# Kernel optimization log

Measured on AMD Instinct MI355X. Metric: run time of the kernel, lower is better.

## Reference

```python
import jax, jax.numpy as jnp
import numpy as np

EXP = 1.4  # cp/cv exponent in the pressure diagnostic

# 2-point stencil primitives (equivalent to the tiny conv3d calls in the torch code)
def bar_x(X):      return 0.5 * (X[:, :, 1:] + X[:, :, :-1])
def dlt_x(X, dx):  return (X[:, :, 1:] - X[:, :, :-1]) / dx
def bar_y(X):      return 0.5 * (X[:, 1:, :] + X[:, :-1, :])
def dlt_y(X, dy):  return (X[:, 1:, :] - X[:, :-1, :]) / dy
def bar_z(X):      return 0.5 * (X[1:] + X[:-1])
def dlt_z(X, dz):  return (X[1:] - X[:-1]) / dz
def pad_x(X):      return jnp.pad(X, ((0, 0), (0, 0), (1, 1)), mode='wrap')      # periodic
def pad_y(X):      return jnp.pad(X, ((0, 0), (1, 1), (0, 0)), mode='wrap')      # periodic
def pad_z(X):      return jnp.pad(X, ((1, 1), (0, 0), (0, 0)))                   # Dirichlet 0 (torch code zeroes top/surface args)


def rhs(U, V, W, Theta, Mu, Phi, dx, dy, dz, PREF, Rd, g):
    u = U / bar_x(pad_x(Mu))                       # (Nz,Ny,Nx+1)
    v = V / bar_y(pad_y(Mu))                       # (Nz,Ny+1,Nx)
    w = W / bar_z(Mu)                              # (Nz-1,Ny,Nx)
    alpha = -dlt_z(pad_z(Phi), dz) / Mu            # (Nz,Ny,Nx)
    theta = Theta / Mu
    p = PREF * (Rd * theta / PREF / alpha) ** EXP
    omega = -w * g / bar_z(alpha) / bar_z(Mu)
    Omega = omega * bar_z(Mu)                      # (Nz-1,Ny,Nx)

    R_U = (-dlt_x(bar_x(pad_x(U)) * bar_x(pad_x(u)), dx)
           - dlt_y(bar_x(pad_x(V)) * bar_y(pad_y(u)), dy)
           - dlt_z(bar_x(pad_x(pad_z(Omega))) * bar_z(pad_z(u)), dz))
    R_V = (-dlt_x(bar_y(pad_y(U)) * bar_x(pad_x(v)), dx)
           - dlt_y(bar_y(pad_y(V)) * bar_y(pad_y(v)), dy)
           - dlt_z(bar_y(pad_y(pad_z(Omega))) * bar_z(pad_z(v)), dz))
    R_W = (-dlt_x(bar_z(U) * bar_x(pad_x(w)), dx)
           - dlt_y(bar_z(V) * bar_y(pad_y(w)), dy)
           - dlt_z(bar_z(pad_z(Omega)) * bar_z(pad_z(w)), dz))
    R_Theta = (-dlt_x(U * bar_x(pad_x(theta)), dx)
               - dlt_y(V * bar_y(pad_y(theta)), dy)
               - dlt_z(pad_z(Omega) * bar_z(pad_z(theta)), dz))
    R_Phi = (-bar_z(bar_x(u)) * dlt_x(bar_x(pad_x(Phi)), dx)
             - bar_z(bar_y(v)) * dlt_y(bar_y(pad_y(Phi)), dy)
             - Omega * dlt_z(bar_z(pad_z(Phi)), dz))
    R_Mu = -dlt_x(U, dx) - dlt_y(V, dy) - dlt_z(pad_z(Omega), dz)

    R_U = R_U + (-bar_x(pad_x(Mu)) * bar_x(pad_x(alpha)) * dlt_x(pad_x(p), dx)
                 - dlt_z(bar_x(bar_z(pad_x(pad_z(p)))), dz) * dlt_x(pad_x(bar_z(pad_z(Phi))), dx))
    R_V = R_V + (-bar_y(pad_y(Mu)) * bar_y(pad_y(alpha)) * dlt_y(pad_y(p), dy)
                 - dlt_z(bar_y(bar_z(pad_y(pad_z(p)))), dz) * dlt_y(pad_y(bar_z(pad_z(Phi))), dy))
    R_W = R_W + g * (dlt_z(p, dz) - bar_z(Mu))
    R_Phi = R_Phi + g * w
    return R_U, R_V, R_W, R_Theta, R_Mu, R_Phi


def rk3_step(U, V, W, Theta, Mu, Phi, dt, dx, dy, dz, PREF, Rd, g):
    rU, rV, rW, rT, rM, rP = rhs(U, V, W, Theta, Mu, Phi, dx, dy, dz, PREF, Rd, g)
    U1, V1, W1 = U + dt * rU / 3, V + dt * rV / 3, W + dt * rW / 3
    T1, M1, P1 = Theta + dt * rT / 3, Mu + dt * rM / 3, Phi + dt * rP / 3
    rU, rV, rW, rT, rM, rP = rhs(U1, V1, W1, T1, M1, P1, dx, dy, dz, PREF, Rd, g)
    U2, V2, W2 = U + dt * rU / 2, V + dt * rV / 2, W + dt * rW / 2
    T2, M2, P2 = Theta + dt * rT / 2, Mu + dt * rM / 2, Phi + dt * rP / 2
    rU, rV, rW, rT, rM, rP = rhs(U2, V2, W2, T2, M2, P2, dx, dy, dz, PREF, Rd, g)
    return (U + dt * rU, V + dt * rV, W + dt * rW,
            Theta + dt * rT, Mu + dt * rM, Phi + dt * rP)


def setup_inputs() -> dict:
    Nz, Ny, Nx = 40, 256, 256
    key = jax.random.key(0)
    k1, k2, k3, k4, k5, k6, k7 = jax.random.split(key, 7)
    dx = dy = dz = 1.0
    dt, PREF, Rd, g = 1e-3, 1.0, 1.0, 0.1

    # Column-mass: positive, O(1)
    Mu = (1.0 + 0.1 * jax.random.uniform(k1, (Nz, Ny, Nx))).astype(jnp.float32)
    # Block-signed vertical diff profile: magnitudes bounded away from 0,
    # distinct block magnitudes so bar_z(alpha) never vanishes at the sign flip.
    base = jnp.where(jnp.arange(Nz) < 30, 1.0, -3.0)[:, None, None]
    d = (base * (1.0 + 0.1 * jax.random.uniform(k2, (Nz, Ny, Nx)))).astype(jnp.float32)
    Phi = jnp.cumsum(d, axis=0)[: Nz - 1]          # (Nz-1,Ny,Nx)
    # alpha exactly as the model will compute it
    alpha = -dlt_z(pad_z(Phi), dz) / Mu            # (Nz,Ny,Nx), sign-definite per block
    s = 1.0 + 0.2 * jax.random.uniform(k3, (Nz, Ny, Nx))
    Theta = ((PREF / Rd) * Mu * alpha * s).astype(jnp.float32)  # theta/alpha = s > 0 -> p well-defined

    U = (0.01 * jax.random.normal(k4, (Nz, Ny, Nx + 1))).astype(jnp.float32)
    V = (0.01 * jax.random.normal(k5, (Nz, Ny + 1, Nx))).astype(jnp.float32)
    W = (0.01 * jax.random.normal(k6, (Nz - 1, Ny, Nx))).astype(jnp.float32)

    bnd = jax.random.uniform(k7, (6, 1, Ny, Nx), dtype=jnp.float32)
    return {"U": U, "V": V, "W": W, "Theta": Theta, "Mu": Mu, "Phi": Phi,
            "Phi_t": bnd[0], "Phi_s": bnd[1], "theta_t": bnd[2], "theta_s": bnd[3],
            "P_t": bnd[4], "P_s": bnd[5],
            "dx": dx, "dy": dy, "dz": dz, "dt": dt, "PREF": PREF, "Rd": Rd, "g": g}


def reference(U, V, W, Theta, Mu, Phi, Phi_t, Phi_s, theta_t, theta_s, P_t, P_s,
              dx, dy, dz, dt, PREF, Rd, g):
    # Phi_t/Phi_s/theta_t/theta_s/P_t/P_s are ignored: the torch pad_z always
    # overwrites top/surface with zeros (faithful to the original code).
    return rk3_step(U, V, W, Theta, Mu, Phi, dt, dx, dy, dz, PREF, Rd, g)
```

## Files before the change

### kernel.cpp

```cpp
#include <hip/hip_runtime.h>
#include <math.h>

#define NZ 40
#define NY 256
#define NX 256
#define NUX 257
#define NYX (NY*NX)
#define KU (NY*NUX)
#define KV ((NY+1)*NX)
#define NUT (NZ*KU)
#define NVT (NZ*KV)
#define NCT (NZ*NYX)
#define NWT ((NZ-1)*NYX)
#define NBLK (NUX*NZ)
#define NHALF (NUT+NVT+NWT+3*NCT+NWT)

typedef _Float16 h16;

__device__ __forceinline__ int ICc(int k,int j,int i){ return (k*NY+j)*NX+i; }
__device__ __forceinline__ int IU (int k,int j,int i){ return (k*NY+j)*NUX+i; }
__device__ __forceinline__ int IV (int k,int j,int i){ return (k*(NY+1)+j)*NX+i; }

__device__ __forceinline__ float fdiv(float a, float b){
  return a * __builtin_amdgcn_rcpf(b);
}
__device__ __forceinline__ float ldh(const h16* __restrict__ a, int idx){
  return (float)a[idx];
}

__global__ __launch_bounds__(256) void diag_all(
    const float* __restrict__ Us, const float* __restrict__ Vs, const float* __restrict__ Ws,
    const float* __restrict__ Ts, const float* __restrict__ Ms, const float* __restrict__ Ps,
    h16* __restrict__ ud, h16* __restrict__ vd, h16* __restrict__ wd,
    h16* __restrict__ thd, h16* __restrict__ ald, h16* __restrict__ pd,
    h16* __restrict__ Omd,
    const float* __restrict__ dzp, const float* __restrict__ PREFp,
    const float* __restrict__ Rdp, const float* __restrict__ gp)
{
  const int i = threadIdx.x;
  const int j = blockIdx.x;
  const int k = blockIdx.y;
  const float rdz = 1.f/(*dzp);
  const float PREF = *PREFp, Rd = *Rdp, g = *gp;
  const float invP = 1.f/PREF;

  const int jj  = j & 255;
  const int jm1 = (j+255) & 255;

  {
    float mjm = Ms[(k*NY+jm1)*NX+i];
    float mjj = Ms[(k*NY+jj )*NX+i];
    const int o = IV(k,j,i);
    vd[o] = (h16)fdiv(Vs[o], 0.5f*(mjm+mjj));
  }

  if (j < NY) {
    const int b = (k*NY+j)*NX;
    float mi  = Ms[b+i];
    float mim = Ms[b+((i+255)&255)];
    ud[IU(k,j,i)] = (h16)fdiv(Us[IU(k,j,i)], 0.5f*(mim+mi));
    if (i == 255) {
      ud[IU(k,j,256)] = (h16)fdiv(Us[IU(k,j,256)], 0.5f*(Ms[b+255]+Ms[b+0]));
    }

    const int c = b + i;
    float mu   = mi;
    float phim = (k>0)    ? Ps[c-NYX] : 0.f;
    float phik = (k<NZ-1) ? Ps[c]     : 0.f;
    float al   = -((phik-phim)*rdz)*__builtin_amdgcn_rcpf(mu);
    float th   = fdiv(Ts[c], mu);
    float x    = Rd*th*invP*__builtin_amdgcn_rcpf(al);
    pd[c]  = (h16)(PREF*__builtin_amdgcn_exp2f(1.4f*__builtin_amdgcn_logf(x)));
    ald[c] = (h16)al;
    thd[c] = (h16)th;
    if (k < NZ-1) {
      float mup  = Ms[c+NYX];
      float phip = (k+1<NZ-1) ? Ps[c+NYX] : 0.f;
      float alp  = -((phip-phik)*rdz)*__builtin_amdgcn_rcpf(mup);
      float muz  = 0.5f*(mu+mup);
      wd[c]  = (h16)fdiv(Ws[c], muz);
      Omd[c] = (h16)(-Ws[c]*g*__builtin_amdgcn_rcpf(muz*(0.5f*(al+alp))));
    }
  }
}

__global__ __launch_bounds__(256,8) void rhs_update(
    const float* __restrict__ Us, const float* __restrict__ Vs,
    const float* __restrict__ Ms, const float* __restrict__ Ps,
    const h16* __restrict__ ud, const h16* __restrict__ vd, const h16* __restrict__ wd,
    const h16* __restrict__ thd, const h16* __restrict__ ald, const h16* __restrict__ pd,
    const h16* __restrict__ Omd,
    const float* __restrict__ Ub, const float* __restrict__ Vb, const float* __restrict__ Wb,
    const float* __restrict__ Tb, const float* __restrict__ Mb, const float* __restrict__ Pb,
    float* __restrict__ Uo, float* __restrict__ Vo, float* __restrict__ Wo,
    float* __restrict__ To, float* __restrict__ Mo, float* __restrict__ Po,
    const float* __restrict__ dxp, const float* __restrict__ dyp, const float* __restrict__ dzp,
    const float* __restrict__ dtp, const float* __restrict__ gp, float cmul)
{
  const int bid = blockIdx.x;
  const int nb  = (bid & 7)*(NBLK/8) + (bid >> 3);
  const int j   = nb / NZ;
  const int k   = nb - NZ*j;
  const int i   = threadIdx.x;

  const float rdx = 1.f/(*dxp), rdy = 1.f/(*dyp), rdz = 1.f/(*dzp);
  const float g = *gp;
  const float c = (*dtp)*cmul;

  const int jj  = j & 255;
  const int jm1 = (j+255) & 255;
  const int jp1c= (j+1) & 255;
  const int im1 = (i+255) & 255;
  const int ip1 = (i+1) & 255;

  auto ru_val = [&](int iu, int iW, int iE)->float {
    const int ii_  = iu & 255;
    const int iim1 = (iu+255) & 255;
    const int bU   = k*KU + j*NUX;

    float ui0 = ldh(ud,bU+iu), uim = ldh(ud,bU+iW), uip = ldh(ud,bU+iE);
    float Uim = Us[bU+iW], Ui0 = Us[bU+iu], Uip = Us[bU+iE];
    float t1 = -(0.25f*(Ui0+Uip)*(ui0+uip) - 0.25f*(Uim+Ui0)*(uim+ui0))*rdx;

    float Vx0 = 0.5f*(Vs[IV(k,j  ,iim1)] + Vs[IV(k,j  ,ii_)]);
    float uy0 = 0.5f*(ldh(ud,IU(k,jm1,iu)) + ui0);
    float Vx1 = 0.5f*(Vs[IV(k,j+1,iim1)] + Vs[IV(k,j+1,ii_)]);
    float uy1 = 0.5f*(ui0 + ldh(ud,IU(k,jp1c,iu)));
    float t2 = -(Vx1*uy1 - Vx0*uy0)*rdy;

    float Omx0 = (k==0)   ? 0.f : 0.5f*(ldh(Omd,ICc(k-1,j,iim1))+ldh(Omd,ICc(k-1,j,ii_)));
    float uz0  = (k==0)   ? 0.5f*ui0 : 0.5f*(ldh(ud,IU(k-1,j,iu))+ui0);
    float Omx1 = (k+1==NZ)? 0.f : 0.5f*(ldh(Omd,ICc(k,j,iim1))+ldh(Omd,ICc(k,j,ii_)));
    float uz1  = (k+1==NZ)? 0.5f*ui0 : 0.5f*(ui0+ldh(ud,IU(k+1,j,iu)));
    float t3 = -(Omx1*uz1 - Omx0*uz0)*rdz;

    float Mux = 0.5f*(Ms[ICc(k,j,iim1)]+Ms[ICc(k,j,ii_)]);
    float alx = 0.5f*(ldh(ald,ICc(k,j,iim1))+ldh(ald,ICc(k,j,ii_)));
    float pt1 = -Mux*alx*(ldh(pd,ICc(k,j,ii_))-ldh(pd,ICc(k,j,iim1)))*rdx;

    auto pzf = [&](int m, int x)->float {
      if (m==0)  return 0.5f*ldh(pd,ICc(0,j,x));
      if (m==NZ) return 0.5f*ldh(pd,ICc(NZ-1,j,x));
      return 0.5f*(ldh(pd,ICc(m-1,j,x))+ldh(pd,ICc(m,j,x)));
    };
    float A = (0.5f*(pzf(k+1,iim1)+pzf(k+1,ii_)) - 0.5f*(pzf(k,iim1)+pzf(k,ii_)))*rdz;
    auto Phzf = [&](int x)->float {
      if (k==0)    return 0.5f*Ps[ICc(0,j,x)];
      if (k==NZ-1) return 0.5f*Ps[ICc(NZ-2,j,x)];
      return 0.5f*(Ps[ICc(k-1,j,x)]+Ps[ICc(k,j,x)]);
    };
    float B = (Phzf(ii_)-Phzf(iim1))*rdx;
    return t1+t2+t3+pt1 + (-A*B);
  };

  if (j < NY) {
    const int iW = i ? (i-1) : 256;
    float rU = ru_val(i, iW, i+1);
    const int o = IU(k,j,i);
    Uo[o] = Ub[o] + c*rU;
    if (i == 255) {
      float rUe = ru_val(256, 255, 0);
      const int oe = IU(k,j,256);
      Uo[oe] = Ub[oe] + c*rUe;
    }
  }

  {
    const int jN = (j==0)   ? 256 : j-1;
    const int jS = (j==256) ? 0   : j+1;
    float vj0 = ldh(vd,IV(k,j,i));
    float vjm = ldh(vd,IV(k,jN,i));
    float vjp = ldh(vd,IV(k,jS,i));
    float Vjm = Vs[IV(k,jN,i)], Vj0 = Vs[IV(k,j,i)], Vjp = Vs[IV(k,jS,i)];
    float t2 = -(0.25f*(Vj0+Vjp)*(vj0+vjp) - 0.25f*(Vjm+Vj0)*(vjm+vj0))*rdy;

    float Uy0 = 0.5f*(Us[IU(k,jm1,i  )] + Us[IU(k,jj,i  )]);
    float vx0 = 0.5f*(ldh(vd,IV(k,j,im1)) + vj0);
    float Uy1 = 0.5f*(Us[IU(k,jm1,i+1)] + Us[IU(k,jj,i+1)]);
    float vx1 = 0.5f*(vj0 + ldh(vd,IV(k,j,ip1)));
    float t1 = -(Uy1*vx1 - Uy0*vx0)*rdx;

    float Omy0 = (k==0)   ? 0.f : 0.5f*(ldh(Omd,ICc(k-1,jm1,i))+ldh(Omd,ICc(k-1,jj,i)));
    float vz0  = (k==0)   ? 0.5f*vj0 : 0.5f*(ldh(vd,IV(k-1,j,i))+vj0);
    float Omy1 = (k+1==NZ)? 0.f : 0.5f*(ldh(Omd,ICc(k,jm1,i))+ldh(Omd,ICc(k,jj,i)));
    float vz1  = (k+1==NZ)? 0.5f*vj0 : 0.5f*(vj0+ldh(vd,IV(k+1,j,i)));
    float t3 = -(Omy1*vz1 - Omy0*vz0)*rdz;

    float Muy = 0.5f*(Ms[ICc(k,jm1,i)]+Ms[ICc(k,jj,i)]);
    float aly = 0.5f*(ldh(ald,ICc(k,jm1,i))+ldh(ald,ICc(k,jj,i)));
    float pt1 = -Muy*aly*(ldh(pd,ICc(k,jj,i))-ldh(pd,ICc(k,jm1,i)))*rdy;

    auto pzfy = [&](int m, int y)->float {
      if (m==0)  return 0.5f*ldh(pd,ICc(0,y,i));
      if (m==NZ) return 0.5f*ldh(pd,ICc(NZ-1,y,i));
      return 0.5f*(ldh(pd,ICc(m-1,y,i))+ldh(pd,ICc(m,y,i)));
    };
    float A = (0.5f*(pzfy(k+1,jm1)+pzfy(k+1,jj)) - 0.5f*(pzfy(k,jm1)+pzfy(k,jj)))*rdz;
    auto Phzfy = [&](int y)->float {
      if (k==0)    return 0.5f*Ps[ICc(0,y,i)];
      if (k==NZ-1) return 0.5f*Ps[ICc(NZ-2,y,i)];
      return 0.5f*(Ps[ICc(k-1,y,i)]+Ps[ICc(k,y,i)]);
    };
    float B = (Phzfy(jj)-Phzfy(jm1))*rdy;
    float pt2 = -A*B;

    const int o = IV(k,j,i);
    Vo[o] = Vb[o] + c*(t1+t2+t3+pt1+pt2);
  }

  if (j < NY) {
    const int cc = ICc(k,j,i);

    float th0 = ldh(thd,cc);
    float thx0 = 0.5f*(ldh(thd,ICc(k,j,im1))+th0);
    float thx1 = 0.5f*(th0+ldh(thd,ICc(k,j,ip1)));
    float s1 = -(Us[IU(k,j,i+1)]*thx1 - Us[IU(k,j,i)]*thx0)*rdx;
    float thy0 = 0.5f*(ldh(thd,ICc(k,jm1,i))+th0);
    float thy1 = 0.5f*(th0+ldh(thd,ICc(k,jp1c,i)));
    float s2 = -(Vs[IV(k,j+1,i)]*thy1 - Vs[IV(k,j,i)]*thy0)*rdy;
    float Om0 = (k==0)    ? 0.f : ldh(Omd,ICc(k-1,j,i));
    float Om1 = (k+1==NZ) ? 0.f : ldh(Omd,cc);
    float thz0 = (k==0)    ? 0.5f*th0 : 0.5f*(ldh(thd,ICc(k-1,j,i))+th0);
    float thz1 = (k+1==NZ) ? 0.5f*th0 : 0.5f*(th0+ldh(thd,ICc(k+1,j,i)));
    float s3 = -(Om1*thz1 - Om0*thz0)*rdz;
    To[cc] = Tb[cc] + c*(s1+s2+s3);

    float rmu = -(Us[IU(k,j,i+1)]-Us[IU(k,j,i)])*rdx
                -(Vs[IV(k,j+1,i)]-Vs[IV(k,j,i)])*rdy
                -(Om1-Om0)*rdz;
    Mo[cc] = Mb[cc] + c*rmu;

    if (k < NZ-1) {
      float w0 = ldh(wd,cc);
      float Uz0 = 0.5f*(Us[IU(k,j,i  )]+Us[IU(k+1,j,i  )]);
      float Uz1 = 0.5f*(Us[IU(k,j,i+1)]+Us[IU(k+1,j,i+1)]);
      float wx0 = 0.5f*(ldh(wd,ICc(k,j,im1))+w0);
      float wx1 = 0.5f*(w0+ldh(wd,ICc(k,j,ip1)));
      float q1 = -(Uz1*wx1 - Uz0*wx0)*rdx;
      float Vz0 = 0.5f*(Vs[IV(k,j  ,i)]+Vs[IV(k+1,j  ,i)]);
      float Vz1 = 0.5f*(Vs[IV(k,j+1,i)]+Vs[IV(k+1,j+1,i)]);
      float wy0 = 0.5f*(ldh(wd,ICc(k,jm1,i))+w0);
      float wy1 = 0.5f*(w0+ldh(wd,ICc(k,jp1c,i)));
      float q2 = -(Vz1*wy1 - Vz0*wy0)*rdy;
      float Omz0 = (k==0)      ? 0.5f*ldh(Omd,ICc(0,j,i))    : 0.5f*(ldh(Omd,ICc(k-1,j,i))+ldh(Omd,cc));
      float wz0  = (k==0)      ? 0.5f*w0 : 0.5f*(ldh(wd,ICc(k-1,j,i))+w0);
      float Omz1 = (k+1==NZ-1) ? 0.5f*ldh(Omd,ICc(NZ-2,j,i)) : 0.5f*(ldh(Omd,cc)+ldh(Omd,ICc(k+1,j,i)));
      float wz1  = (k+1==NZ-1) ? 0.5f*w0 : 0.5f*(w0+ldh(wd,ICc(k+1,j,i)));
      float q3 = -(Omz1*wz1 - Omz0*wz0)*rdz;
      float pw = g*((ldh(pd,ICc(k+1,j,i))-ldh(pd,cc))*rdz - 0.5f*(Ms[cc]+Ms[ICc(k+1,j,i)]));
      Wo[cc] = Wb[cc] + c*(q1+q2+q3+pw);

      float ux0 = 0.5f*(ldh(ud,IU(k  ,j,i))+ldh(ud,IU(k  ,j,i+1)));
      float ux1 = 0.5f*(ldh(ud,IU(k+1,j,i))+ldh(ud,IU(k+1,j,i+1)));
      float uzx = 0.5f*(ux0+ux1);
      float dPhx = 0.5f*(Ps[ICc(k,j,ip1)]-Ps[ICc(k,j,im1)])*rdx;
      float vy0 = 0.5f*(ldh(vd,IV(k  ,j,i))+ldh(vd,IV(k  ,j+1,i)));
      float vy1 = 0.5f*(ldh(vd,IV(k+1,j,i))+ldh(vd,IV(k+1,j+1,i)));
      float vzy = 0.5f*(vy0+vy1);
      float dPhy = 0.5f*(Ps[ICc(k,jp1c,i)]-Ps[ICc(k,jm1,i)])*rdy;
      float Phz0 = (k==0)      ? 0.5f*Ps[ICc(0,j,i)]    : 0.5f*(Ps[ICc(k-1,j,i)]+Ps[cc]);
      float Phz1 = (k+1==NZ-1) ? 0.5f*Ps[ICc(NZ-2,j,i)] : 0.5f*(Ps[cc]+Ps[ICc(k+1,j,i)]);
      float p3 = -ldh(Omd,cc)*(Phz1-Phz0)*rdz;
      Po[cc] = Pb[cc] + c*(-uzx*dPhx - vzy*dPhy + p3 + g*w0);
    }
  }
}

extern "C" void kernel_launch(void* const* d_in, const int* in_sizes, int n_in,
                              void* d_out, int out_size, void* d_ws, size_t ws_size,
                              hipStream_t stream)
{
  const float* U = (const float*)d_in[0];
  const float* V = (const float*)d_in[1];
  const float* W = (const float*)d_in[2];
  const float* T = (const float*)d_in[3];
  const float* M = (const float*)d_in[4];
  const float* P = (const float*)d_in[5];
  const float* dxp  = (const float*)d_in[12];
  const float* dyp  = (const float*)d_in[13];
  const float* dzp  = (const float*)d_in[14];
  const float* dtp  = (const float*)d_in[15];
  const float* PREFp= (const float*)d_in[16];
  const float* Rdp  = (const float*)d_in[17];
  const float* gp   = (const float*)d_in[18];

  h16* hw = (h16*)d_ws;
  h16* ud  = hw;         h16* vd  = ud +NUT;  h16* wd = vd +NVT;
  h16* thd = wd +NWT;    h16* ald = thd+NCT;  h16* pd = ald+NCT;
  h16* Omd = pd +NCT;
  float* S = (float*)(hw + NHALF);
  float* SU=S; float* SV=SU+NUT; float* SW=SV+NVT; float* ST=SW+NWT; float* SM=ST+NCT; float* SP=SM+NCT;

  float* o = (float*)d_out;
  float* OU=o; float* OV=OU+NUT; float* OW=OV+NVT; float* OT=OW+NWT; float* OM=OT+NCT; float* OP=OM+NCT;

  dim3 dblk(256,1,1), dgrd(NUX, NZ, 1);
  dim3 rblk(256,1,1), rgrd(NBLK, 1, 1);

  auto stage = [&](const float* sU,const float* sV,const float* sW,
                   const float* sT,const float* sM,const float* sP,
                   float* oU,float* oV,float* oW,float* oT,float* oM,float* oP,
                   float cmul){
    hipLaunchKernelGGL(diag_all, dgrd, dblk, 0, stream,
                       sU,sV,sW,sT,sM,sP, ud,vd,wd,thd,ald,pd,Omd, dzp,PREFp,Rdp,gp);
    hipLaunchKernelGGL(rhs_update, rgrd, rblk, 0, stream,
                       sU,sV,sM,sP, ud,vd,wd,thd,ald,pd,Omd,
                       U,V,W,T,M,P, oU,oV,oW,oT,oM,oP,
                       dxp,dyp,dzp,dtp,gp, cmul);
  };

  stage(U,V,W,T,M,P,          OU,OV,OW,OT,OM,OP, 1.f/3.f);
  stage(OU,OV,OW,OT,OM,OP,    SU,SV,SW,ST,SM,SP, 0.5f   );
  stage(SU,SV,SW,ST,SM,SP,    OU,OV,OW,OT,OM,OP, 1.f    );
}
```

Baseline: 311.7 us.

## Stage neighbor stencil rows in LDS and lower rhs_update occupancy target

Each block now cooperatively loads every neighbor row it needs (the half-precision u, v, w, theta, p, Omega and alpha fields plus the float Phi and Mu rows) into shared memory once, then computes all stencil terms from LDS. This replaces repeated, partly shifted global loads. The k==0 and k==NZ-1 branches disappear because out-of-range rows are stored as zeros. The launch-bounds minimum-blocks hint also drops from 8 to 6 to relax register pressure. In exchange it adds a block-wide barrier and about 40 staging loads per thread before any compute, which may serialize memory latency that was previously overlapped.

```diff
diff --git a/kernel.cpp b/kernel.cpp
--- a/kernel.cpp
+++ b/kernel.cpp
@@ -84,7 +84,7 @@
   }
 }
 
-__global__ __launch_bounds__(256,8) void rhs_update(
+__global__ __launch_bounds__(256,6) void rhs_update(
     const float* __restrict__ Us, const float* __restrict__ Vs,
     const float* __restrict__ Ms, const float* __restrict__ Ps,
     const h16* __restrict__ ud, const h16* __restrict__ vd, const h16* __restrict__ wd,
@@ -107,49 +107,84 @@
   const float g = *gp;
   const float c = (*dtp)*cmul;
 
-  const int jj  = j & 255;
-  const int jm1 = (j+255) & 255;
-  const int jp1c= (j+1) & 255;
-  const int im1 = (i+255) & 255;
-  const int ip1 = (i+1) & 255;
+  const int jj   = j & 255;
+  const int jm1  = (j+255) & 255;
+  const int jp1m = (j+1) & 255;
+  const int im1  = (i+255) & 255;
+  const int ip1  = (i+1) & 255;
+  const int jN   = (j==0)   ? 256 : j-1;
+  const int jS   = (j==256) ? 0   : j+1;
+
+  __shared__ h16  Lud[5][258];
+  __shared__ h16  Lvd[6][256];
+  __shared__ h16  Lwd[5][256];
+  __shared__ h16  Lth[5][256];
+  __shared__ h16  Lpd[6][256];
+  __shared__ h16  LOm[5][256];
+  __shared__ h16  Lal[2][256];
+  __shared__ float LPs[6][256];
+  __shared__ float LMs[3][256];
+
+#define STC(dst,src,kk,jr,kmax) dst[i] = ((unsigned)(kk)<(unsigned)(kmax)) ? src[((kk)*NY+(jr))*NX+i] : (h16)0.f
+#define STF(dst,src,kk,jr,kmax) dst[i] = ((unsigned)(kk)<(unsigned)(kmax)) ? src[((kk)*NY+(jr))*NX+i] : 0.f
+#define STU(dst,kk,jr) do{ bool v_=((unsigned)(kk)<(unsigned)NZ); \
+    dst[i] = v_ ? ud[((kk)*NY+(jr))*NUX+i] : (h16)0.f; \
+    if (i==0) dst[256] = v_ ? ud[((kk)*NY+(jr))*NUX+256] : (h16)0.f; }while(0)
+#define STV(dst,kk,jr) dst[i] = ((unsigned)(kk)<(unsigned)NZ) ? vd[((kk)*(NY+1)+(jr))*NX+i] : (h16)0.f
+
+  STU(Lud[0],k,  jm1); STU(Lud[1],k,  jj ); STU(Lud[2],k,  jp1m);
+  STU(Lud[3],k-1,jj ); STU(Lud[4],k+1,jj );
+  STV(Lvd[0],k,  jN ); STV(Lvd[1],k,  j  ); STV(Lvd[2],k,  jS );
+  STV(Lvd[3],k-1,j  ); STV(Lvd[4],k+1,j  ); STV(Lvd[5],k+1,jS );
+  STC(Lwd[0],wd,k,  jm1,NZ-1); STC(Lwd[1],wd,k,  jj ,NZ-1); STC(Lwd[2],wd,k,  jp1m,NZ-1);
+  STC(Lwd[3],wd,k-1,jj ,NZ-1); STC(Lwd[4],wd,k+1,jj ,NZ-1);
+  STC(Lth[0],thd,k,  jm1,NZ); STC(Lth[1],thd,k,  jj ,NZ); STC(Lth[2],thd,k,  jp1m,NZ);
+  STC(Lth[3],thd,k-1,jj ,NZ); STC(Lth[4],thd,k+1,jj ,NZ);
+  STC(Lpd[0],pd,k-1,jj ,NZ); STC(Lpd[1],pd,k,  jj ,NZ); STC(Lpd[2],pd,k+1,jj ,NZ);
+  STC(Lpd[3],pd,k-1,jm1,NZ); STC(Lpd[4],pd,k,  jm1,NZ); STC(Lpd[5],pd,k+1,jm1,NZ);
+  STC(LOm[0],Omd,k-1,jj ,NZ-1); STC(LOm[1],Omd,k,  jj ,NZ-1); STC(LOm[2],Omd,k+1,jj ,NZ-1);
+  STC(LOm[3],Omd,k-1,jm1,NZ-1); STC(LOm[4],Omd,k,  jm1,NZ-1);
+  Lal[0][i] = ald[(k*NY+jj )*NX+i];
+  Lal[1][i] = ald[(k*NY+jm1)*NX+i];
+  STF(LPs[0],Ps,k-1,jj ,NZ-1); STF(LPs[1],Ps,k,  jj ,NZ-1); STF(LPs[2],Ps,k+1,jj ,NZ-1);
+  STF(LPs[3],Ps,k,  jm1,NZ-1); STF(LPs[4],Ps,k,  jp1m,NZ-1); STF(LPs[5],Ps,k-1,jm1,NZ-1);
+  STF(LMs[0],Ms,k,  jm1,NZ); STF(LMs[1],Ms,k,  jj ,NZ); STF(LMs[2],Ms,k+1,jj ,NZ);
+
+  __syncthreads();
 
   auto ru_val = [&](int iu, int iW, int iE)->float {
     const int ii_  = iu & 255;
     const int iim1 = (iu+255) & 255;
     const int bU   = k*KU + j*NUX;
 
-    float ui0 = ldh(ud,bU+iu), uim = ldh(ud,bU+iW), uip = ldh(ud,bU+iE);
+    float ui0 = (float)Lud[1][iu], uim = (float)Lud[1][iW], uip = (float)Lud[1][iE];
     float Uim = Us[bU+iW], Ui0 = Us[bU+iu], Uip = Us[bU+iE];
     float t1 = -(0.25f*(Ui0+Uip)*(ui0+uip) - 0.25f*(Uim+Ui0)*(uim+ui0))*rdx;
 
     float Vx0 = 0.5f*(Vs[IV(k,j  ,iim1)] + Vs[IV(k,j  ,ii_)]);
-    float uy0 = 0.5f*(ldh(ud,IU(k,jm1,iu)) + ui0);
+    float uy0 = 0.5f*((float)Lud[0][iu] + ui0);
     float Vx1 = 0.5f*(Vs[IV(k,j+1,iim1)] + Vs[IV(k,j+1,ii_)]);
-    float uy1 = 0.5f*(ui0 + ldh(ud,IU(k,jp1c,iu)));
+    float uy1 = 0.5f*(ui0 + (float)Lud[2][iu]);
     float t2 = -(Vx1*uy1 - Vx0*uy0)*rdy;
 
-    float Omx0 = (k==0)   ? 0.f : 0.5f*(ldh(Omd,ICc(k-1,j,iim1))+ldh(Omd,ICc(k-1,j,ii_)));
-    float uz0  = (k==0)   ? 0.5f*ui0 : 0.5f*(ldh(ud,IU(k-1,j,iu))+ui0);
-    float Omx1 = (k+1==NZ)? 0.f : 0.5f*(ldh(Omd,ICc(k,j,iim1))+ldh(Omd,ICc(k,j,ii_)));
-    float uz1  = (k+1==NZ)? 0.5f*ui0 : 0.5f*(ui0+ldh(ud,IU(k+1,j,iu)));
+    float Omx0 = 0.5f*((float)LOm[0][iim1]+(float)LOm[0][ii_]);
+    float uz0  = 0.5f*((float)Lud[3][iu] + ui0);
+    float Omx1 = 0.5f*((float)LOm[1][iim1]+(float)LOm[1][ii_]);
+    float uz1  = 0.5f*(ui0 + (float)Lud[4][iu]);
     float t3 = -(Omx1*uz1 - Omx0*uz0)*rdz;
 
-    float Mux = 0.5f*(Ms[ICc(k,j,iim1)]+Ms[ICc(k,j,ii_)]);
-    float alx = 0.5f*(ldh(ald,ICc(k,j,iim1))+ldh(ald,ICc(k,j,ii_)));
-    float pt1 = -Mux*alx*(ldh(pd,ICc(k,j,ii_))-ldh(pd,ICc(k,j,iim1)))*rdx;
-
-    auto pzf = [&](int m, int x)->float {
-      if (m==0)  return 0.5f*ldh(pd,ICc(0,j,x));
-      if (m==NZ) return 0.5f*ldh(pd,ICc(NZ-1,j,x));
-      return 0.5f*(ldh(pd,ICc(m-1,j,x))+ldh(pd,ICc(m,j,x)));
-    };
-    float A = (0.5f*(pzf(k+1,iim1)+pzf(k+1,ii_)) - 0.5f*(pzf(k,iim1)+pzf(k,ii_)))*rdz;
-    auto Phzf = [&](int x)->float {
-      if (k==0)    return 0.5f*Ps[ICc(0,j,x)];
-      if (k==NZ-1) return 0.5f*Ps[ICc(NZ-2,j,x)];
-      return 0.5f*(Ps[ICc(k-1,j,x)]+Ps[ICc(k,j,x)]);
-    };
-    float B = (Phzf(ii_)-Phzf(iim1))*rdx;
+    float Mux = 0.5f*(LMs[1][iim1]+LMs[1][ii_]);
+    float alx = 0.5f*((float)Lal[0][iim1]+(float)Lal[0][ii_]);
+    float pt1 = -Mux*alx*((float)Lpd[1][ii_]-(float)Lpd[1][iim1])*rdx;
+
+    float pzk_m  = 0.5f*((float)Lpd[0][iim1]+(float)Lpd[1][iim1]);
+    float pzk_c  = 0.5f*((float)Lpd[0][ii_ ]+(float)Lpd[1][ii_ ]);
+    float pzk1_m = 0.5f*((float)Lpd[1][iim1]+(float)Lpd[2][iim1]);
+    float pzk1_c = 0.5f*((float)Lpd[1][ii_ ]+(float)Lpd[2][ii_ ]);
+    float A = (0.5f*(pzk1_m+pzk1_c) - 0.5f*(pzk_m+pzk_c))*rdz;
+    float Phz_m = 0.5f*(LPs[0][iim1]+LPs[1][iim1]);
+    float Phz_c = 0.5f*(LPs[0][ii_ ]+LPs[1][ii_ ]);
+    float B = (Phz_c-Phz_m)*rdx;
     return t1+t2+t3+pt1 + (-A*B);
   };
 
@@ -166,42 +201,36 @@
   }
 
   {
-    const int jN = (j==0)   ? 256 : j-1;
-    const int jS = (j==256) ? 0   : j+1;
-    float vj0 = ldh(vd,IV(k,j,i));
-    float vjm = ldh(vd,IV(k,jN,i));
-    float vjp = ldh(vd,IV(k,jS,i));
+    float vj0 = (float)Lvd[1][i];
+    float vjm = (float)Lvd[0][i];
+    float vjp = (float)Lvd[2][i];
     float Vjm = Vs[IV(k,jN,i)], Vj0 = Vs[IV(k,j,i)], Vjp = Vs[IV(k,jS,i)];
     float t2 = -(0.25f*(Vj0+Vjp)*(vj0+vjp) - 0.25f*(Vjm+Vj0)*(vjm+vj0))*rdy;
 
     float Uy0 = 0.5f*(Us[IU(k,jm1,i  )] + Us[IU(k,jj,i  )]);
-    float vx0 = 0.5f*(ldh(vd,IV(k,j,im1)) + vj0);
+    float vx0 = 0.5f*((float)Lvd[1][im1] + vj0);
     float Uy1 = 0.5f*(Us[IU(k,jm1,i+1)] + Us[IU(k,jj,i+1)]);
-    float vx1 = 0.5f*(vj0 + ldh(vd,IV(k,j,ip1)));
+    float vx1 = 0.5f*(vj0 + (float)Lvd[1][ip1]);
     float t1 = -(Uy1*vx1 - Uy0*vx0)*rdx;
 
-    float Omy0 = (k==0)   ? 0.f : 0.5f*(ldh(Omd,ICc(k-1,jm1,i))+ldh(Omd,ICc(k-1,jj,i)));
-    float vz0  = (k==0)   ? 0.5f*vj0 : 0.5f*(ldh(vd,IV(k-1,j,i))+vj0);
-    float Omy1 = (k+1==NZ)? 0.f : 0.5f*(ldh(Omd,ICc(k,jm1,i))+ldh(Omd,ICc(k,jj,i)));
-    float vz1  = (k+1==NZ)? 0.5f*vj0 : 0.5f*(vj0+ldh(vd,IV(k+1,j,i)));
+    float Omy0 = 0.5f*((float)LOm[3][i]+(float)LOm[0][i]);
+    float vz0  = 0.5f*((float)Lvd[3][i]+vj0);
+    float Omy1 = 0.5f*((float)LOm[4][i]+(float)LOm[1][i]);
+    float vz1  = 0.5f*(vj0+(float)Lvd[4][i]);
     float t3 = -(Omy1*vz1 - Omy0*vz0)*rdz;
 
-    float Muy = 0.5f*(Ms[ICc(k,jm1,i)]+Ms[ICc(k,jj,i)]);
-    float aly = 0.5f*(ldh(ald,ICc(k,jm1,i))+ldh(ald,ICc(k,jj,i)));
-    float pt1 = -Muy*aly*(ldh(pd,ICc(k,jj,i))-ldh(pd,ICc(k,jm1,i)))*rdy;
-
-    auto pzfy = [&](int m, int y)->float {
-      if (m==0)  return 0.5f*ldh(pd,ICc(0,y,i));
-      if (m==NZ) return 0.5f*ldh(pd,ICc(NZ-1,y,i));
-      return 0.5f*(ldh(pd,ICc(m-1,y,i))+ldh(pd,ICc(m,y,i)));
-    };
-    float A = (0.5f*(pzfy(k+1,jm1)+pzfy(k+1,jj)) - 0.5f*(pzfy(k,jm1)+pzfy(k,jj)))*rdz;
-    auto Phzfy = [&](int y)->float {
-      if (k==0)    return 0.5f*Ps[ICc(0,y,i)];
-      if (k==NZ-1) return 0.5f*Ps[ICc(NZ-2,y,i)];
-      return 0.5f*(Ps[ICc(k-1,y,i)]+Ps[ICc(k,y,i)]);
-    };
-    float B = (Phzfy(jj)-Phzfy(jm1))*rdy;
+    float Muy = 0.5f*(LMs[0][i]+LMs[1][i]);
+    float aly = 0.5f*((float)Lal[1][i]+(float)Lal[0][i]);
+    float pt1 = -Muy*aly*((float)Lpd[1][i]-(float)Lpd[4][i])*rdy;
+
+    float pzk_m  = 0.5f*((float)Lpd[3][i]+(float)Lpd[4][i]);
+    float pzk_c  = 0.5f*((float)Lpd[0][i]+(float)Lpd[1][i]);
+    float pzk1_m = 0.5f*((float)Lpd[4][i]+(float)Lpd[5][i]);
+    float pzk1_c = 0.5f*((float)Lpd[1][i]+(float)Lpd[2][i]);
+    float A = (0.5f*(pzk1_m+pzk1_c) - 0.5f*(pzk_m+pzk_c))*rdz;
+    float Phy_c = 0.5f*(LPs[0][i]+LPs[1][i]);
+    float Phy_m = 0.5f*(LPs[5][i]+LPs[3][i]);
+    float B = (Phy_c-Phy_m)*rdy;
     float pt2 = -A*B;
 
     const int o = IV(k,j,i);
@@ -211,17 +240,17 @@
   if (j < NY) {
     const int cc = ICc(k,j,i);
 
-    float th0 = ldh(thd,cc);
-    float thx0 = 0.5f*(ldh(thd,ICc(k,j,im1))+th0);
-    float thx1 = 0.5f*(th0+ldh(thd,ICc(k,j,ip1)));
+    float th0 = (float)Lth[1][i];
+    float thx0 = 0.5f*((float)Lth[1][im1]+th0);
+    float thx1 = 0.5f*(th0+(float)Lth[1][ip1]);
     float s1 = -(Us[IU(k,j,i+1)]*thx1 - Us[IU(k,j,i)]*thx0)*rdx;
-    float thy0 = 0.5f*(ldh(thd,ICc(k,jm1,i))+th0);
-    float thy1 = 0.5f*(th0+ldh(thd,ICc(k,jp1c,i)));
+    float thy0 = 0.5f*((float)Lth[0][i]+th0);
+    float thy1 = 0.5f*(th0+(float)Lth[2][i]);
     float s2 = -(Vs[IV(k,j+1,i)]*thy1 - Vs[IV(k,j,i)]*thy0)*rdy;
-    float Om0 = (k==0)    ? 0.f : ldh(Omd,ICc(k-1,j,i));
-    float Om1 = (k+1==NZ) ? 0.f : ldh(Omd,cc);
-    float thz0 = (k==0)    ? 0.5f*th0 : 0.5f*(ldh(thd,ICc(k-1,j,i))+th0);
-    float thz1 = (k+1==NZ) ? 0.5f*th0 : 0.5f*(th0+ldh(thd,ICc(k+1,j,i)));
+    float Om0 = (float)LOm[0][i];
+    float Om1 = (float)LOm[1][i];
+    float thz0 = 0.5f*((float)Lth[3][i]+th0);
+    float thz1 = 0.5f*(th0+(float)Lth[4][i]);
     float s3 = -(Om1*thz1 - Om0*thz0)*rdz;
     To[cc] = Tb[cc] + c*(s1+s2+s3);
 
@@ -231,39 +260,43 @@
     Mo[cc] = Mb[cc] + c*rmu;
 
     if (k < NZ-1) {
-      float w0 = ldh(wd,cc);
+      float w0 = (float)Lwd[1][i];
       float Uz0 = 0.5f*(Us[IU(k,j,i  )]+Us[IU(k+1,j,i  )]);
       float Uz1 = 0.5f*(Us[IU(k,j,i+1)]+Us[IU(k+1,j,i+1)]);
-      float wx0 = 0.5f*(ldh(wd,ICc(k,j,im1))+w0);
-      float wx1 = 0.5f*(w0+ldh(wd,ICc(k,j,ip1)));
+      float wx0 = 0.5f*((float)Lwd[1][im1]+w0);
+      float wx1 = 0.5f*(w0+(float)Lwd[1][ip1]);
       float q1 = -(Uz1*wx1 - Uz0*wx0)*rdx;
       float Vz0 = 0.5f*(Vs[IV(k,j  ,i)]+Vs[IV(k+1,j  ,i)]);
       float Vz1 = 0.5f*(Vs[IV(k,j+1,i)]+Vs[IV(k+1,j+1,i)]);
-      float wy0 = 0.5f*(ldh(wd,ICc(k,jm1,i))+w0);
-      float wy1 = 0.5f*(w0+ldh(wd,ICc(k,jp1c,i)));
+      float wy0 = 0.5f*((float)Lwd[0][i]+w0);
+      float wy1 = 0.5f*(w0+(float)Lwd[2][i]);
       float q2 = -(Vz1*wy1 - Vz0*wy0)*rdy;
-      float Omz0 = (k==0)      ? 0.5f*ldh(Omd,ICc(0,j,i))    : 0.5f*(ldh(Omd,ICc(k-1,j,i))+ldh(Omd,cc));
-      float wz0  = (k==0)      ? 0.5f*w0 : 0.5f*(ldh(wd,ICc(k-1,j,i))+w0);
-      float Omz1 = (k+1==NZ-1) ? 0.5f*ldh(Omd,ICc(NZ-2,j,i)) : 0.5f*(ldh(Omd,cc)+ldh(Omd,ICc(k+1,j,i)));
-      float wz1  = (k+1==NZ-1) ? 0.5f*w0 : 0.5f*(w0+ldh(wd,ICc(k+1,j,i)));
+      float Omz0 = 0.5f*((float)LOm[0][i]+(float)LOm[1][i]);
+      float wz0  = 0.5f*((float)Lwd[3][i]+w0);
+      float Omz1 = 0.5f*((float)LOm[1][i]+(float)LOm[2][i]);
+      float wz1  = 0.5f*(w0+(float)Lwd[4][i]);
       float q3 = -(Omz1*wz1 - Omz0*wz0)*rdz;
-      float pw = g*((ldh(pd,ICc(k+1,j,i))-ldh(pd,cc))*rdz - 0.5f*(Ms[cc]+Ms[ICc(k+1,j,i)]));
+      float pw = g*(((float)Lpd[2][i]-(float)Lpd[1][i])*rdz - 0.5f*(LMs[1][i]+LMs[2][i]));
       Wo[cc] = Wb[cc] + c*(q1+q2+q3+pw);
 
-      float ux0 = 0.5f*(ldh(ud,IU(k  ,j,i))+ldh(ud,IU(k  ,j,i+1)));
-      float ux1 = 0.5f*(ldh(ud,IU(k+1,j,i))+ldh(ud,IU(k+1,j,i+1)));
+      float ux0 = 0.5f*((float)Lud[1][i]+(float)Lud[1][i+1]);
+      float ux1 = 0.5f*((float)Lud[4][i]+(float)Lud[4][i+1]);
       float uzx = 0.5f*(ux0+ux1);
-      float dPhx = 0.5f*(Ps[ICc(k,j,ip1)]-Ps[ICc(k,j,im1)])*rdx;
-      float vy0 = 0.5f*(ldh(vd,IV(k  ,j,i))+ldh(vd,IV(k  ,j+1,i)));
-      float vy1 = 0.5f*(ldh(vd,IV(k+1,j,i))+ldh(vd,IV(k+1,j+1,i)));
+      float dPhx = 0.5f*(LPs[1][ip1]-LPs[1][im1])*rdx;
+      float vy0 = 0.5f*((float)Lvd[1][i]+(float)Lvd[2][i]);
+      float vy1 = 0.5f*((float)Lvd[4][i]+(float)Lvd[5][i]);
       float vzy = 0.5f*(vy0+vy1);
-      float dPhy = 0.5f*(Ps[ICc(k,jp1c,i)]-Ps[ICc(k,jm1,i)])*rdy;
-      float Phz0 = (k==0)      ? 0.5f*Ps[ICc(0,j,i)]    : 0.5f*(Ps[ICc(k-1,j,i)]+Ps[cc]);
-      float Phz1 = (k+1==NZ-1) ? 0.5f*Ps[ICc(NZ-2,j,i)] : 0.5f*(Ps[cc]+Ps[ICc(k+1,j,i)]);
-      float p3 = -ldh(Omd,cc)*(Phz1-Phz0)*rdz;
+      float dPhy = 0.5f*(LPs[4][i]-LPs[3][i])*rdy;
+      float Phz0 = 0.5f*(LPs[0][i]+LPs[1][i]);
+      float Phz1 = 0.5f*(LPs[1][i]+LPs[2][i]);
+      float p3 = -(float)LOm[1][i]*(Phz1-Phz0)*rdz;
       Po[cc] = Pb[cc] + c*(-uzx*dPhx - vzy*dPhy + p3 + g*w0);
     }
   }
+#undef STC
+#undef STF
+#undef STU
+#undef STV
 }
 
 extern "C" void kernel_launch(void* const* d_in, const int* in_sizes, int n_in,
```

Result: slower. 386.7 us (+24.1%).
